# Kernel optimization log

Measured on AMD Instinct MI355X. Metric: run time of the kernel, lower is better.

The kernel has to match this reference:

```python
import jax, jax.numpy as jnp
import numpy as np

B, T, D, H = 64, 257, 1024, 16
F = 4096
R = 16
HD = D // H


def _layer_norm(x, g, b, eps=1e-5):
    mu = x.mean(-1, keepdims=True)
    var = x.var(-1, keepdims=True)
    return (x - mu) / jnp.sqrt(var + eps) * g + b


def _quick_gelu(x):
    return x * jax.nn.sigmoid(1.702 * x)


def _attention(x, Wq, bq, Wk, bk, Wv, bv, Wo, bo):
    scale = HD ** -0.5
    q = (x @ Wq + bq) * scale
    k = x @ Wk + bk
    v = x @ Wv + bv
    q = q.reshape(B, T, H, HD).transpose(0, 2, 1, 3)
    k = k.reshape(B, T, H, HD).transpose(0, 2, 1, 3)
    v = v.reshape(B, T, H, HD).transpose(0, 2, 1, 3)
    attn = jax.nn.softmax(jnp.einsum('bhqd,bhkd->bhqk', q, k), axis=-1)
    o = jnp.einsum('bhqk,bhkd->bhqd', attn, v)
    o = o.transpose(0, 2, 1, 3).reshape(B, T, D)
    return o @ Wo + bo


def _match_indices(metric, r, class_token=True):
    # cosine-normalized bipartite matching (no-grad path in torch; index-only here)
    m = metric / jnp.linalg.norm(metric, axis=-1, keepdims=True)
    a, b = m[:, ::2, :], m[:, 1::2, :]        # [B, ta, D], [B, tb, D]
    scores = jnp.einsum('nac,nbc->nab', a, b)  # [B, ta, tb]
    if class_token:
        scores = scores.at[:, 0, :].set(-jnp.inf)
    node_max = scores.max(-1)
    node_idx = scores.argmax(-1)
    edge_idx = jnp.argsort(-node_max, axis=-1)  # descending
    unm_idx = edge_idx[:, r:]
    src_idx = edge_idx[:, :r]
    dst_idx = jnp.take_along_axis(node_idx, src_idx, axis=-1)
    if class_token:
        unm_idx = jnp.sort(unm_idx, axis=1)
    return unm_idx, src_idx, dst_idx


def _merge_sum(x, unm_idx, src_idx, dst_idx):
    src, dst = x[:, ::2, :], x[:, 1::2, :]
    c = x.shape[-1]
    unm = jnp.take_along_axis(src, unm_idx[..., None], axis=1)       # [B, ta-r, c]
    sel = jnp.take_along_axis(src, src_idx[..., None], axis=1)       # [B, r, c]
    dst = jax.vmap(lambda d, di, sv: d.at[di].add(sv))(dst, dst_idx, sel)
    return jnp.concatenate([unm, dst], axis=1)                       # [B, T-r, c]


def setup_inputs() -> dict:
    key = jax.random.key(0)
    ks = jax.random.split(key, 12)
    s = 0.02
    return {
        'hidden_states': jax.random.normal(ks[0], (B, T, D), jnp.float32),
        'ln1_g': jnp.ones((D,), jnp.float32),
        'ln1_b': jnp.zeros((D,), jnp.float32),
        'Wq': jax.random.normal(ks[1], (D, D), jnp.float32) * s,
        'bq': jnp.zeros((D,), jnp.float32),
        'Wk': jax.random.normal(ks[2], (D, D), jnp.float32) * s,
        'bk': jnp.zeros((D,), jnp.float32),
        'Wv': jax.random.normal(ks[3], (D, D), jnp.float32) * s,
        'bv': jnp.zeros((D,), jnp.float32),
        'Wo': jax.random.normal(ks[4], (D, D), jnp.float32) * s,
        'bo': jnp.zeros((D,), jnp.float32),
        'ln2_g': jnp.ones((D,), jnp.float32),
        'ln2_b': jnp.zeros((D,), jnp.float32),
        'W1': jax.random.normal(ks[5], (D, F), jnp.float32) * s,
        'b1': jnp.zeros((F,), jnp.float32),
        'W2': jax.random.normal(ks[6], (F, D), jnp.float32) * s,
        'b2': jnp.zeros((D,), jnp.float32),
    }


def reference(hidden_states, ln1_g, ln1_b, Wq, bq, Wk, bk, Wv, bv, Wo, bo,
              ln2_g, ln2_b, W1, b1, W2, b2):
    # 1) LN1 + self-attention + residual
    x = hidden_states + _attention(_layer_norm(hidden_states, ln1_g, ln1_b),
                                   Wq, bq, Wk, bk, Wv, bv, Wo, bo)
    # 2) ToMe merge with weighted average (initial size = ones -> merge_wavg)
    metric = jax.lax.stop_gradient(x)
    unm_idx, src_idx, dst_idx = _match_indices(metric, R, class_token=True)
    size = jnp.ones((B, T, 1), x.dtype)
    x = _merge_sum(x * size, unm_idx, src_idx, dst_idx)
    size = _merge_sum(size, unm_idx, src_idx, dst_idx)
    x = x / size
    # 3) LN2 + MLP (quick_gelu) + residual
    h = _layer_norm(x, ln2_g, ln2_b)
    h = _quick_gelu(h @ W1 + b1) @ W2 + b2
    return x + h  # [B, T - R, D]
```

## Files before the change

### kernel.cpp

```cpp
#include <hip/hip_runtime.h>
#include <math.h>

#define BB 64
#define TT 257
#define DD 1024
#define HH 16
#define FF 4096
#define RR 16
#define HDD 64
#define TMM 241
#define M1 (BB*TT)
#define M2 (BB*TMM)
#define NA 129
#define NB 128

typedef float f4v __attribute__((ext_vector_type(4)));
typedef short s8v __attribute__((ext_vector_type(8)));
typedef short s4v __attribute__((ext_vector_type(4)));
typedef unsigned short us;

__device__ __forceinline__ us f2bf(float f){
  unsigned u = __float_as_uint(f);
  u += 0x7fffu + ((u >> 16) & 1u);
  return (us)(u >> 16);
}
__device__ __forceinline__ float bf2f(us h){
  return __uint_as_float(((unsigned)h) << 16);
}
__device__ __forceinline__ void gl16(const us* g, us* l){
  __builtin_amdgcn_global_load_lds((const __attribute__((address_space(1))) void*)g,
                                   (__attribute__((address_space(3))) void*)l, 16, 0, 0);
}

__global__ __launch_bounds__(64) void lnstats_kernel(const float* __restrict__ x,
                                                     float* __restrict__ st)
{
  int row = blockIdx.x, lane = threadIdx.x;
  const float* p = x + (size_t)row * DD;
  float s = 0.0f, sq = 0.0f;
  #pragma unroll
  for (int i = 0; i < 4; i++){
    float4 v = *(const float4*)(p + i * 256 + lane * 4);
    s  += v.x + v.y + v.z + v.w;
    sq += v.x*v.x + v.y*v.y + v.z*v.z + v.w*v.w;
  }
  #pragma unroll
  for (int m = 1; m < 64; m <<= 1){ s += __shfl_xor(s, m); sq += __shfl_xor(sq, m); }
  if (lane == 0){
    float mu  = s * (1.0f / DD);
    float var = sq * (1.0f / DD) - mu * mu;
    st[2*row]     = mu;
    st[2*row + 1] = 1.0f / sqrtf(var + 1e-5f);
  }
}

__global__ __launch_bounds__(256) void lncvt_kernel(const float* __restrict__ x,
    const float* __restrict__ st, const float* __restrict__ g,
    const float* __restrict__ b, us* __restrict__ out)
{
  int row = blockIdx.x, tid = threadIdx.x;
  float mu = st[2*row], rstd = st[2*row + 1];
  float4 xv = *(const float4*)(x + (size_t)row * DD + tid * 4);
  float4 gv = *(const float4*)(g + tid * 4);
  float4 bv = *(const float4*)(b + tid * 4);
  s4v o;
  o[0] = (short)f2bf((xv.x - mu) * rstd * gv.x + bv.x);
  o[1] = (short)f2bf((xv.y - mu) * rstd * gv.y + bv.y);
  o[2] = (short)f2bf((xv.z - mu) * rstd * gv.z + bv.z);
  o[3] = (short)f2bf((xv.w - mu) * rstd * gv.w + bv.w);
  *(s4v*)(out + (size_t)row * DD + tid * 4) = o;
}

__global__ __launch_bounds__(256) void wt_kernel(const float* __restrict__ src,
                                                 us* __restrict__ dhi,
                                                 us* __restrict__ dlo,
                                                 int K, int N)
{
  __shared__ float t[32][33];
  int tx = threadIdx.x, ty = threadIdx.y;
  int n0 = blockIdx.x * 32, k0 = blockIdx.y * 32;
  #pragma unroll
  for (int r = 0; r < 4; r++)
    t[ty + 8*r][tx] = src[(size_t)(k0 + ty + 8*r) * N + n0 + tx];
  __syncthreads();
  #pragma unroll
  for (int r = 0; r < 4; r++){
    float f = t[tx][ty + 8*r];
    us hi = f2bf(f);
    size_t o = (size_t)(n0 + ty + 8*r) * K + k0 + tx;
    dhi[o] = hi;
    if (dlo) dlo[o] = f2bf(f - bf2f(hi));
  }
}

__global__ __launch_bounds__(256) void qkv_kernel(const float* __restrict__ hidden,
    const us* __restrict__ WBh, const us* __restrict__ WBl,
    const float* __restrict__ bq, const float* __restrict__ bk, const float* __restrict__ bv,
    const float* __restrict__ lnstat, const float* __restrict__ lng, const float* __restrict__ lnb,
    us* __restrict__ qhp, us* __restrict__ qlp, us* __restrict__ khp,
    us* __restrict__ klp, us* __restrict__ vhp, us* __restrict__ vlp)
{
  const int M = M1, K = DD;
  __shared__ __align__(16) us Ah[128*32];
  __shared__ __align__(16) us Bh[128*32];
  __shared__ __align__(16) us Al[128*32];
  __shared__ __align__(16) us Bl[128*32];
  int tid = threadIdx.x;
  int m0 = blockIdx.y * 128, n0 = blockIdx.x * 128;
  int lane = tid & 63, w = tid >> 6;
  int wr = w >> 1, wc = w & 1;
  int fr = lane & 15, fq = lane >> 4;
  f4v acc[4][4];
  f4v zero = {0.0f, 0.0f, 0.0f, 0.0f};
  #pragma unroll
  for (int i = 0; i < 4; i++)
    #pragma unroll
    for (int j = 0; j < 4; j++) acc[i][j] = zero;
  int srow = tid >> 1, sseg = (tid & 1) * 16;
  int arow0 = m0 + srow; if (arow0 >= M) arow0 = M - 1;
  float mu = lnstat[2*arow0], rstd = lnstat[2*arow0 + 1];
  int lr = lane >> 2, lc = (lane & 3) * 8;
  int gb0 = n0 + w*32 + lr;

  for (int kk = 0; kk < K; kk += 32){
    {
      const float* ap = hidden + (size_t)arow0 * K + kk + sseg;
      #pragma unroll
      for (int i = 0; i < 4; i++){
        float4 f = *(const float4*)(ap + 4*i);
        float4 gv = *(const float4*)(lng + kk + sseg + 4*i);
        float4 bv2 = *(const float4*)(lnb + kk + sseg + 4*i);
        f.x = (f.x - mu) * rstd * gv.x + bv2.x;
        f.y = (f.y - mu) * rstd * gv.y + bv2.y;
        f.z = (f.z - mu) * rstd * gv.z + bv2.z;
        f.w = (f.w - mu) * rstd * gv.w + bv2.w;
        s4v h;
        h[0] = (short)f2bf(f.x); h[1] = (short)f2bf(f.y);
        h[2] = (short)f2bf(f.z); h[3] = (short)f2bf(f.w);
        *(s4v*)&Ah[srow*32 + sseg + 4*i] = h;
        s4v l;
        l[0] = (short)f2bf(f.x - bf2f((us)h[0]));
        l[1] = (short)f2bf(f.y - bf2f((us)h[1]));
        l[2] = (short)f2bf(f.z - bf2f((us)h[2]));
        l[3] = (short)f2bf(f.w - bf2f((us)h[3]));
        *(s4v*)&Al[srow*32 + sseg + 4*i] = l;
      }
    }
    gl16(WBh + (size_t)gb0 * K + kk + lc,        &Bh[(w*32)*32]);
    gl16(WBh + (size_t)(gb0 + 16) * K + kk + lc, &Bh[(w*32 + 16)*32]);
    gl16(WBl + (size_t)gb0 * K + kk + lc,        &Bl[(w*32)*32]);
    gl16(WBl + (size_t)(gb0 + 16) * K + kk + lc, &Bl[(w*32 + 16)*32]);
    __syncthreads();
    s8v ah[4], bh[4], al[4], bl[4];
    #pragma unroll
    for (int m = 0; m < 4; m++){
      ah[m] = *(const s8v*)&Ah[(wr*64 + m*16 + fr)*32 + fq*8];
      al[m] = *(const s8v*)&Al[(wr*64 + m*16 + fr)*32 + fq*8];
    }
    #pragma unroll
    for (int n = 0; n < 4; n++){
      bh[n] = *(const s8v*)&Bh[(wc*64 + n*16 + fr)*32 + fq*8];
      bl[n] = *(const s8v*)&Bl[(wc*64 + n*16 + fr)*32 + fq*8];
    }
    #pragma unroll
    for (int m = 0; m < 4; m++)
      #pragma unroll
      for (int n = 0; n < 4; n++){
        acc[m][n] = __builtin_amdgcn_mfma_f32_16x16x32_bf16(ah[m], bh[n], acc[m][n], 0, 0, 0);
        acc[m][n] = __builtin_amdgcn_mfma_f32_16x16x32_bf16(ah[m], bl[n], acc[m][n], 0, 0, 0);
        acc[m][n] = __builtin_amdgcn_mfma_f32_16x16x32_bf16(al[m], bh[n], acc[m][n], 0, 0, 0);
      }
    __syncthreads();
  }
  int kind = n0 >> 10;
  const float* bsel = (kind == 0) ? bq : (kind == 1) ? bk : bv;
  us* C0 = (kind == 0) ? qhp : (kind == 1) ? khp : vhp;
  us* C1 = (kind == 0) ? qlp : (kind == 1) ? klp : vlp;
  float scl = (kind == 0) ? 0.125f : 1.0f;
  #pragma unroll
  for (int m = 0; m < 4; m++){
    int grow0 = m0 + wr*64 + m*16 + fq*4;
    #pragma unroll
    for (int n = 0; n < 4; n++){
      int gcol = n0 + wc*64 + n*16 + fr;
      int lcn = gcol & 1023;
      int h2 = lcn >> 6, d2 = lcn & 63;
      float bcol = bsel[lcn];
      #pragma unroll
      for (int i = 0; i < 4; i++){
        int grow = grow0 + i;
        if (grow < M){
          int b2 = grow / 257;
          int t2 = grow - b2 * 257;
          size_t off2 = ((size_t)(b2*16 + h2) * 257 + t2) * 64 + d2;
          float v = (acc[m][n][i] + bcol) * scl;
          us hi = f2bf(v);
          C0[off2] = hi;
          C1[off2] = f2bf(v - bf2f(hi));
        }
      }
    }
  }
}

template<int AMODE, int SPLIT, int EPI>
__global__ __launch_bounds__(256) void gemm2_kernel(const us* __restrict__ Ahp,
    const us* __restrict__ Alp,
    const us* __restrict__ BTh, const us* __restrict__ BTl,
    const float* __restrict__ bias, const float* __restrict__ resid,
    void* __restrict__ C0, int M, int N, int K)
{
  __shared__ __align__(16) us Ah[128*32];
  __shared__ __align__(16) us Bh[128*32];
  __shared__ __align__(16) us Al[SPLIT ? 128*32 : 8];
  __shared__ __align__(16) us Bl[SPLIT ? 128*32 : 8];
  int tid = threadIdx.x;
  int m0 = blockIdx.y * 128, n0 = blockIdx.x * 128;
  int lane = tid & 63, w = tid >> 6;
  int wr = w >> 1, wc = w & 1;
  int fr = lane & 15, fq = lane >> 4;
  f4v acc[4][4];
  f4v zero = {0.0f, 0.0f, 0.0f, 0.0f};
  #pragma unroll
  for (int i = 0; i < 4; i++)
    #pragma unroll
    for (int j = 0; j < 4; j++) acc[i][j] = zero;
  int lr = lane >> 2, lc = (lane & 3) * 8;
  int ga0 = m0 + w*32 + lr;      if (ga0 >= M) ga0 = M - 1;
  int ga1 = m0 + w*32 + 16 + lr; if (ga1 >= M) ga1 = M - 1;
  int gb0 = n0 + w*32 + lr;
  int b2a = ga0 / 257, t2a = ga0 - b2a * 257;
  int b2b = ga1 / 257, t2b = ga1 - b2b * 257;

  for (int kk = 0; kk < K; kk += 32){
    if (AMODE == 1){
      gl16(Ahp + (size_t)ga0 * K + kk + lc, &Ah[(w*32)*32]);
      gl16(Ahp + (size_t)ga1 * K + kk + lc, &Ah[(w*32 + 16)*32]);
      if (SPLIT){
        gl16(Alp + (size_t)ga0 * K + kk + lc, &Al[(w*32)*32]);
        gl16(Alp + (size_t)ga1 * K + kk + lc, &Al[(w*32 + 16)*32]);
      }
    } else {
      int h2 = kk >> 6, d2 = (kk & 63) + lc;
      size_t o0 = ((size_t)(b2a*16 + h2) * 257 + t2a) * 64 + d2;
      size_t o1 = ((size_t)(b2b*16 + h2) * 257 + t2b) * 64 + d2;
      gl16(Ahp + o0, &Ah[(w*32)*32]);
      gl16(Ahp + o1, &Ah[(w*32 + 16)*32]);
      if (SPLIT){
        gl16(Alp + o0, &Al[(w*32)*32]);
        gl16(Alp + o1, &Al[(w*32 + 16)*32]);
      }
    }
    gl16(BTh + (size_t)gb0 * K + kk + lc,        &Bh[(w*32)*32]);
    gl16(BTh + (size_t)(gb0 + 16) * K + kk + lc, &Bh[(w*32 + 16)*32]);
    if (SPLIT){
      gl16(BTl + (size_t)gb0 * K + kk + lc,        &Bl[(w*32)*32]);
      gl16(BTl + (size_t)(gb0 + 16) * K + kk + lc, &Bl[(w*32 + 16)*32]);
    }
    __syncthreads();
    s8v ah[4], bh[4], al[4], bl[4];
    #pragma unroll
    for (int m = 0; m < 4; m++){
      ah[m] = *(const s8v*)&Ah[(wr*64 + m*16 + fr)*32 + fq*8];
      if (SPLIT) al[m] = *(const s8v*)&Al[(wr*64 + m*16 + fr)*32 + fq*8];
    }
    #pragma unroll
    for (int n = 0; n < 4; n++){
      bh[n] = *(const s8v*)&Bh[(wc*64 + n*16 + fr)*32 + fq*8];
      if (SPLIT) bl[n] = *(const s8v*)&Bl[(wc*64 + n*16 + fr)*32 + fq*8];
    }
    #pragma unroll
    for (int m = 0; m < 4; m++)
      #pragma unroll
      for (int n = 0; n < 4; n++){
        acc[m][n] = __builtin_amdgcn_mfma_f32_16x16x32_bf16(ah[m], bh[n], acc[m][n], 0, 0, 0);
        if (SPLIT){
          acc[m][n] = __builtin_amdgcn_mfma_f32_16x16x32_bf16(ah[m], bl[n], acc[m][n], 0, 0, 0);
          acc[m][n] = __builtin_amdgcn_mfma_f32_16x16x32_bf16(al[m], bh[n], acc[m][n], 0, 0, 0);
        }
      }
    __syncthreads();
  }
  #pragma unroll
  for (int m = 0; m < 4; m++){
    int grow0 = m0 + wr*64 + m*16 + fq*4;
    #pragma unroll
    for (int n = 0; n < 4; n++){
      int gcol = n0 + wc*64 + n*16 + fr;
      float bcol = bias[gcol];
      #pragma unroll
      for (int i = 0; i < 4; i++){
        int grow = grow0 + i;
        if (grow < M){
          float v = acc[m][n][i] + bcol;
          size_t off = (size_t)grow * N + gcol;
          if (EPI == 1){
            ((float*)C0)[off] = v + resid[off];
          } else {
            float gq = v / (1.0f + expf(-1.702f * v));
            ((us*)C0)[off] = f2bf(gq);
          }
        }
      }
    }
  }
}

__global__ __launch_bounds__(512, 1) void attn_flash_kernel(
    const us* __restrict__ Qh, const us* __restrict__ Ql,
    const us* __restrict__ Kh, const us* __restrict__ Klo,
    const us* __restrict__ Vh, const us* __restrict__ Vlo,
    us* Oh, us* Ol)
{
  __shared__ __align__(16) us Kl[257 * 128];
  __shared__ __align__(16) us Vl[64 * 640];
  int bh = blockIdx.x;
  const size_t hb = (size_t)bh * 257 * 64;
  int tid = threadIdx.x;
  int l = tid & 63, w = tid >> 6;
  int g = l >> 4, c = l & 15;
  const float NEG = -3.0e38f;

  {
    s8v z8 = {0,0,0,0,0,0,0,0};
    for (int idx = tid; idx < 64*640/8; idx += 512)
      *((s8v*)Vl + idx) = z8;
  }
  __syncthreads();
  for (int idx = tid; idx < 257*8; idx += 512){
    int tok = idx >> 3, ch = idx & 7;
    int sw = (tok & 7) << 4;
    s8v hv = *(const s8v*)(Kh  + hb + (size_t)tok * 64 + ch*8);
    s8v lv = *(const s8v*)(Klo + hb + (size_t)tok * 64 + ch*8);
    char* kr = (char*)Kl + tok * 256;
    *(s8v*)(kr + ((ch*16) ^ sw)) = hv;
    *(s8v*)(kr + 128 + ((ch*16) ^ sw)) = lv;
  }
  for (int idx = tid; idx < 257*8; idx += 512){
    int tok = idx >> 3, ch = idx & 7;
    s8v hv = *(const s8v*)(Vh  + hb + (size_t)tok * 64 + ch*8);
    s8v lv = *(const s8v*)(Vlo + hb + (size_t)tok * 64 + ch*8);
    #pragma unroll
    for (int j = 0; j < 8; j++){
      int d = ch*8 + j;
      char* vr = (char*)Vl + d * 1280;
      int off = (tok * 2) ^ (j << 4);
      *(us*)(vr + off) = (us)hv[j];
      *(us*)(vr + 640 + off) = (us)lv[j];
    }
  }
  __syncthreads();

  for (int qt = w; qt < 17; qt += 8){
    int t0 = qt * 16;
    int qr = t0 + c; if (qr > 256) qr = 256;
    const us* qp  = Qh + hb + (size_t)qr * 64 + g*8;
    const us* qp2 = Ql + hb + (size_t)qr * 64 + g*8;
    s8v qhi[2], qlo[2];
    qhi[0] = *(const s8v*)(qp);       qhi[1] = *(const s8v*)(qp + 32);
    qlo[0] = *(const s8v*)(qp2);      qlo[1] = *(const s8v*)(qp2 + 32);

    float m_run = NEG, l_run = 0.0f;
    f4v o4[4];
    #pragma unroll
    for (int dt = 0; dt < 4; dt++) o4[dt] = (f4v){0.0f, 0.0f, 0.0f, 0.0f};

    #pragma unroll 1
    for (int mck = 0; mck < 9; mck++){
      f4v a0, a1;
      {
        int t = 2*mck;
        int krow = t * 16 + c; if (krow > 256) krow = 256;
        char* kr = (char*)Kl + krow * 256;
        int sw = (krow & 7) << 4;
        s8v khi0 = *(const s8v*)(kr + ((g * 16) ^ sw));
        s8v khi1 = *(const s8v*)(kr + ((64 + g * 16) ^ sw));
        s8v klo0 = *(const s8v*)(kr + 128 + ((g * 16) ^ sw));
        s8v klo1 = *(const s8v*)(kr + 128 + ((64 + g * 16) ^ sw));
        f4v a = {0.0f, 0.0f, 0.0f, 0.0f};
        a = __builtin_amdgcn_mfma_f32_16x16x32_bf16(khi0, qhi[0], a, 0, 0, 0);
        a = __builtin_amdgcn_mfma_f32_16x16x32_bf16(khi1, qhi[1], a, 0, 0, 0);
        a = __builtin_amdgcn_mfma_f32_16x16x32_bf16(khi0, qlo[0], a, 0, 0, 0);
        a = __builtin_amdgcn_mfma_f32_16x16x32_bf16(khi1, qlo[1], a, 0, 0, 0);
        a = __builtin_amdgcn_mfma_f32_16x16x32_bf16(klo0, qhi[0], a, 0, 0, 0);
        a = __builtin_amdgcn_mfma_f32_16x16x32_bf16(klo1, qhi[1], a, 0, 0, 0);
        a0 = a;
      }
      if (mck < 8){
        int t = 2*mck + 1;
        int krow = t * 16 + c; if (krow > 256) krow = 256;
        char* kr = (char*)Kl + krow * 256;
        int sw = (krow & 7) << 4;
        s8v khi0 = *(const s8v*)(kr + ((g * 16) ^ sw));
        s8v khi1 = *(const s8v*)(kr + ((64 + g * 16) ^ sw));
        s8v klo0 = *(const s8v*)(kr + 128 + ((g * 16) ^ sw));
        s8v klo1 = *(const s8v*)(kr + 128 + ((64 + g * 16) ^ sw));
        f4v a = {0.0f, 0.0f, 0.0f, 0.0f};
        a = __builtin_amdgcn_mfma_f32_16x16x32_bf16(khi0, qhi[0], a, 0, 0, 0);
        a = __builtin_amdgcn_mfma_f32_16x16x32_bf16(khi1, qhi[1], a, 0, 0, 0);
        a = __builtin_amdgcn_mfma_f32_16x16x32_bf16(khi0, qlo[0], a, 0, 0, 0);
        a = __builtin_amdgcn_mfma_f32_16x16x32_bf16(khi1, qlo[1], a, 0, 0, 0);
        a = __builtin_amdgcn_mfma_f32_16x16x32_bf16(klo0, qhi[0], a, 0, 0, 0);
        a = __builtin_amdgcn_mfma_f32_16x16x32_bf16(klo1, qhi[1], a, 0, 0, 0);
        a1 = a;
      } else {
        a1 = (f4v){NEG, NEG, NEG, NEG};
        a0[0] = (g == 0) ? a0[0] : NEG;
        a0[1] = NEG; a0[2] = NEG; a0[3] = NEG;
      }
      float cm = fmaxf(fmaxf(fmaxf(a0[0], a0[1]), fmaxf(a0[2], a0[3])),
                       fmaxf(fmaxf(a1[0], a1[1]), fmaxf(a1[2], a1[3])));
      cm = fmaxf(cm, __shfl_xor(cm, 16));
      cm = fmaxf(cm, __shfl_xor(cm, 32));
      float m_new = fmaxf(m_run, cm);
      float scl = __expf(m_run - m_new);
      m_run = m_new;
      l_run *= scl;
      #pragma unroll
      for (int dt = 0; dt < 4; dt++){
        o4[dt][0] *= scl; o4[dt][1] *= scl; o4[dt][2] *= scl; o4[dt][3] *= scl;
      }
      float ls = 0.0f;
      unsigned Ph2[2][2], Pl2[2][2];
      #pragma unroll
      for (int k2 = 0; k2 < 2; k2++){
        float e0 = __expf(a0[2*k2] - m_new), e1 = __expf(a0[2*k2+1] - m_new);
        ls += e0 + e1;
        us h0 = f2bf(e0), h1 = f2bf(e1);
        Ph2[0][k2] = (unsigned)h0 | ((unsigned)h1 << 16);
        Pl2[0][k2] = (unsigned)f2bf(e0 - bf2f(h0)) | ((unsigned)f2bf(e1 - bf2f(h1)) << 16);
        float e2 = __expf(a1[2*k2] - m_new), e3 = __expf(a1[2*k2+1] - m_new);
        ls += e2 + e3;
        us h2 = f2bf(e2), h3 = f2bf(e3);
        Ph2[1][k2] = (unsigned)h2 | ((unsigned)h3 << 16);
        Pl2[1][k2] = (unsigned)f2bf(e2 - bf2f(h2)) | ((unsigned)f2bf(e3 - bf2f(h3)) << 16);
      }
      l_run += ls;
      s8v pbh, pbl;
      #pragma unroll
      for (int ww = 0; ww < 4; ww++){
        int srcl = (((g & 1) * 2 + (ww >> 1)) << 4) | c;
        unsigned h0 = (unsigned)__shfl((int)Ph2[0][ww & 1], srcl, 64);
        unsigned lo0 = (unsigned)__shfl((int)Pl2[0][ww & 1], srcl, 64);
        unsigned h1 = (unsigned)__shfl((int)Ph2[1][ww & 1], srcl, 64);
        unsigned lo1 = (unsigned)__shfl((int)Pl2[1][ww & 1], srcl, 64);
        ((unsigned*)&pbh)[ww] = (g >> 1) ? h1 : h0;
        ((unsigned*)&pbl)[ww] = (g >> 1) ? lo1 : lo0;
      }
      #pragma unroll
      for (int dt = 0; dt < 4; dt++){
        int d = dt * 16 + c;
        char* vr = (char*)Vl + d * 1280;
        int off = (mck * 64 + g * 16) ^ ((d & 7) << 4);
        s8v vh = *(const s8v*)(vr + off);
        s8v vlo = *(const s8v*)(vr + 640 + off);
        o4[dt] = __builtin_amdgcn_mfma_f32_16x16x32_bf16(vh, pbh, o4[dt], 0, 0, 0);
        o4[dt] = __builtin_amdgcn_mfma_f32_16x16x32_bf16(vh, pbl, o4[dt], 0, 0, 0);
        o4[dt] = __builtin_amdgcn_mfma_f32_16x16x32_bf16(vlo, pbh, o4[dt], 0, 0, 0);
      }
    }
    l_run += __shfl_xor(l_run, 16);
    l_run += __shfl_xor(l_run, 32);
    float inv = 1.0f / l_run;
    int qrow = t0 + c;
    if (qrow <= 256){
      us* oph = Oh + hb + (size_t)qrow * 64;
      us* opl = Ol + hb + (size_t)qrow * 64;
      #pragma unroll
      for (int dt = 0; dt < 4; dt++){
        s4v hv4, lv4;
        #pragma unroll
        for (int i = 0; i < 4; i++){
          float ov = o4[dt][i] * inv;
          us hi = f2bf(ov);
          hv4[i] = (short)hi;
          lv4[i] = (short)f2bf(ov - bf2f(hi));
        }
        *(s4v*)(oph + dt*16 + g*4) = hv4;
        *(s4v*)(opl + dt*16 + g*4) = lv4;
      }
    }
  }
}

__global__ __launch_bounds__(64) void norms_kernel(const float* __restrict__ x, float* __restrict__ nrm)
{
  int row = blockIdx.x, lane = threadIdx.x;
  const float* p = x + (size_t)row * DD;
  float sq = 0.0f;
  #pragma unroll
  for (int i = 0; i < 4; i++){
    float4 v = *(const float4*)(p + i * 256 + lane * 4);
    sq += v.x*v.x + v.y*v.y + v.z*v.z + v.w*v.w;
  }
  #pragma unroll
  for (int m = 1; m < 64; m <<= 1) sq += __shfl_xor(sq, m);
  if (lane == 0) nrm[row] = sqrtf(sq);
}

__global__ __launch_bounds__(256) void scores_kernel(const float* __restrict__ x,
                                                     const float* __restrict__ nrm,
                                                     float* __restrict__ sc)
{
  __shared__ __align__(16) float as_[16][1028];
  __shared__ __align__(16) float bs_[16][1028];
  int it = blockIdx.x, b = blockIdx.y;
  int tid = threadIdx.x;
  int rloc = tid >> 4, chunk = tid & 15;
  {
    int i = it * 16 + rloc;
    int tg = (i < NA) ? 2 * i : 2 * (NA - 1);
    const float* p = x + ((size_t)b * TT + tg) * DD + chunk * 64;
    #pragma unroll
    for (int ii = 0; ii < 16; ii++)
      *(float4*)&as_[rloc][chunk * 64 + 4*ii] = *(const float4*)(p + 4*ii);
  }
  for (int jt = 0; jt < 8; jt++){
    __syncthreads();
    {
      int j = jt * 16 + rloc;
      const float* p = x + ((size_t)b * TT + 2*j + 1) * DD + chunk * 64;
      #pragma unroll
      for (int ii = 0; ii < 16; ii++)
        *(float4*)&bs_[rloc][chunk * 64 + 4*ii] = *(const float4*)(p + 4*ii);
    }
    __syncthreads();
    int iloc = tid >> 4, jloc = tid & 15;
    float sum = 0.0f;
    #pragma unroll 8
    for (int cgg = 0; cgg < 1024; cgg += 4){
      float4 av = *(const float4*)&as_[iloc][cgg];
      float4 bvv = *(const float4*)&bs_[jloc][cgg];
      sum += av.x*bvv.x + av.y*bvv.y + av.z*bvv.z + av.w*bvv.w;
    }
    int i = it * 16 + iloc, j = jt * 16 + jloc;
    if (i < NA){
      float val = sum / (nrm[(size_t)b * TT + 2*i] * nrm[(size_t)b * TT + 2*j + 1]);
      sc[((size_t)b * NA + i) * NB + j] = val;
    }
  }
}

__global__ __launch_bounds__(64) void node_kernel(const float* __restrict__ sc,
                                                  float* __restrict__ nmax, int* __restrict__ nidx)
{
  int i = blockIdx.x, b = blockIdx.y, lane = threadIdx.x;
  const float* row = sc + ((size_t)b * NA + i) * NB;
  float v0 = row[lane];
  float v1 = row[lane + 64];
  float bv = v0; int bi = lane;
  if (v1 > bv){ bv = v1; bi = lane + 64; }
  #pragma unroll
  for (int m = 1; m < 64; m <<= 1){
    float ov = __shfl_xor(bv, m);
    int oi = __shfl_xor(bi, m);
    if (ov > bv || (ov == bv && oi < bi)){ bv = ov; bi = oi; }
  }
  if (lane == 0){
    if (i == 0){ nmax[(size_t)b * NA] = -INFINITY; nidx[(size_t)b * NA] = 0; }
    else { nmax[(size_t)b * NA + i] = bv; nidx[(size_t)b * NA + i] = bi; }
  }
}

__global__ __launch_bounds__(256) void rank_kernel(const float* __restrict__ nmax,
    const int* __restrict__ nidx, int* __restrict__ src, int* __restrict__ dst,
    int* __restrict__ unm, int* __restrict__ cnt)
{
  __shared__ float v[NA];
  __shared__ int rk[NA];
  __shared__ int edge[NA];
  __shared__ int cs[NB];
  int b = blockIdx.x, t = threadIdx.x;
  if (t < NA) v[t] = nmax[(size_t)b * NA + t];
  if (t < NB) cs[t] = 0;
  __syncthreads();
  if (t < NA){
    float vt = v[t]; int r = 0;
    for (int i = 0; i < NA; i++){
      float vi = v[i];
      r += (vi > vt) || (vi == vt && i < t);
    }
    rk[t] = r; edge[r] = t;
  }
  __syncthreads();
  if (t < RR){
    int s = edge[t];
    src[b * RR + t] = s;
    int d = nidx[(size_t)b * NA + s];
    dst[b * RR + t] = d;
    atomicAdd(&cs[d], 1);
  }
  if (t < NA && rk[t] >= RR){
    int p = 0;
    for (int i = 0; i < NA; i++) p += (i < t) && (rk[i] >= RR);
    unm[b * (NA - RR) + p] = t;
  }
  __syncthreads();
  if (t < NB) cnt[b * NB + t] = cs[t];
}

__global__ __launch_bounds__(256) void merge_kernel(const float* __restrict__ x,
    const int* __restrict__ src, const int* __restrict__ dst, const int* __restrict__ unm,
    const int* __restrict__ cnt, float* __restrict__ xm)
{
  int u = blockIdx.x, b = blockIdx.y;
  int c = threadIdx.x * 4;
  const float* xb = x + (size_t)b * TT * DD;
  float4 acc;
  if (u < NA - RR){
    int ts = 2 * unm[b * (NA - RR) + u];
    acc = *(const float4*)(xb + (size_t)ts * DD + c);
  } else {
    int j = u - (NA - RR);
    acc = *(const float4*)(xb + (size_t)(2*j + 1) * DD + c);
    #pragma unroll
    for (int k2 = 0; k2 < RR; k2++){
      if (dst[b * RR + k2] == j){
        int ts = 2 * src[b * RR + k2];
        float4 av = *(const float4*)(xb + (size_t)ts * DD + c);
        acc.x += av.x; acc.y += av.y; acc.z += av.z; acc.w += av.w;
      }
    }
    float inv = 1.0f / (float)(1 + cnt[b * NB + j]);
    acc.x *= inv; acc.y *= inv; acc.z *= inv; acc.w *= inv;
  }
  *(float4*)(xm + ((size_t)b * TMM + u) * DD + c) = acc;
}

extern "C" void kernel_launch(void* const* d_in, const int* in_sizes, int n_in,
                              void* d_out, int out_size, void* d_ws, size_t ws_size,
                              hipStream_t stream)
{
  (void)in_sizes; (void)n_in; (void)out_size; (void)ws_size;
  const float* hidden = (const float*)d_in[0];
  const float* ln1_g  = (const float*)d_in[1];
  const float* ln1_b  = (const float*)d_in[2];
  const float* Wq = (const float*)d_in[3];
  const float* bq = (const float*)d_in[4];
  const float* Wk = (const float*)d_in[5];
  const float* bk = (const float*)d_in[6];
  const float* Wv = (const float*)d_in[7];
  const float* bv = (const float*)d_in[8];
  const float* Wo = (const float*)d_in[9];
  const float* bo = (const float*)d_in[10];
  const float* ln2_g = (const float*)d_in[11];
  const float* ln2_b = (const float*)d_in[12];
  const float* W1 = (const float*)d_in[13];
  const float* b1 = (const float*)d_in[14];
  const float* W2 = (const float*)d_in[15];
  const float* b2 = (const float*)d_in[16];

  char* base = (char*)d_ws;
  const size_t PE = (size_t)M1 * DD;
  const size_t PL = PE * sizeof(us);
  us* qh = (us*)base;          us* ql = qh + PE;
  us* kh = (us*)(base + 2*PL); us* kl = kh + PE;
  us* vh = (us*)(base + 4*PL); us* vl = vh + PE;
  us* wts = (us*)(base + 6*PL);
  const size_t WD = (size_t)DD * DD;
  us* wqh = wts;
  us* wkh = wqh + WD;
  us* wvh = wkh + WD;
  us* wql = wvh + WD;
  us* wkl = wql + WD;
  us* wvl = wkl + WD;
  us* woh = wvl + WD;
  us* wol = woh + WD;
  us* w1h = wol + WD;
  us* w2h = w1h + (size_t)DD * FF;
  float* lnst1 = (float*)(w2h + (size_t)FF * DD);
  float* xb = (float*)(base + 2*PL);
  float* nrm   = (float*)(base + 4*PL);
  float* sc    = nrm + M1;
  float* nmaxp = sc + (size_t)BB * NA * NB;
  int*   nidxp = (int*)(nmaxp + BB * NA);
  int*   srcI  = nidxp + BB * NA;
  int*   dstI  = srcI + BB * RR;
  int*   unmI  = dstI + BB * RR;
  int*   cntI  = unmI + BB * (NA - RR);
  us*    xh2   = (us*)(base + 4*PL + (size_t)8*1024*1024);
  float* lnst2 = (float*)(base + 4*PL + (size_t)48*1024*1024);
  float* xm = (float*)d_out;
  us* mid = (us*)base;

  dim3 tb32(32, 8);
  wt_kernel<<<dim3(DD/32, DD/32), tb32, 0, stream>>>(Wq, wqh, wql, DD, DD);
  wt_kernel<<<dim3(DD/32, DD/32), tb32, 0, stream>>>(Wk, wkh, wkl, DD, DD);
  wt_kernel<<<dim3(DD/32, DD/32), tb32, 0, stream>>>(Wv, wvh, wvl, DD, DD);
  wt_kernel<<<dim3(DD/32, DD/32), tb32, 0, stream>>>(Wo, woh, wol, DD, DD);
  wt_kernel<<<dim3(FF/32, DD/32), tb32, 0, stream>>>(W1, w1h, nullptr, DD, FF);
  wt_kernel<<<dim3(DD/32, FF/32), tb32, 0, stream>>>(W2, w2h, nullptr, FF, DD);

  lnstats_kernel<<<M1, 64, 0, stream>>>(hidden, lnst1);

  qkv_kernel<<<dim3(3072/128, (M1 + 127)/128), 256, 0, stream>>>(hidden, wqh, wql,
      bq, bk, bv, lnst1, ln1_g, ln1_b, qh, ql, kh, kl, vh, vl);

  attn_flash_kernel<<<BB*HH, 512, 0, stream>>>(qh, ql, kh, kl, vh, vl, qh, ql);

  gemm2_kernel<2,1,1><<<dim3(DD/128, (M1 + 127)/128), 256, 0, stream>>>(qh, ql, woh, wol,
      bo, hidden, xb, M1, DD, DD);

  norms_kernel<<<M1, 64, 0, stream>>>(xb, nrm);
  scores_kernel<<<dim3(9, BB), 256, 0, stream>>>(xb, nrm, sc);
  node_kernel<<<dim3(NA, BB), 64, 0, stream>>>(sc, nmaxp, nidxp);
  rank_kernel<<<BB, 256, 0, stream>>>(nmaxp, nidxp, srcI, dstI, unmI, cntI);
  merge_kernel<<<dim3(TMM, BB), 256, 0, stream>>>(xb, srcI, dstI, unmI, cntI, xm);

  lnstats_kernel<<<M2, 64, 0, stream>>>(xm, lnst2);
  lncvt_kernel<<<M2, 256, 0, stream>>>(xm, lnst2, ln2_g, ln2_b, xh2);

  gemm2_kernel<1,0,2><<<dim3(FF/128, (M2 + 127)/128), 256, 0, stream>>>(xh2, nullptr, w1h, nullptr,
      b1, nullptr, mid, M2, FF, DD);
  gemm2_kernel<1,0,1><<<dim3(DD/128, (M2 + 127)/128), 256, 0, stream>>>(mid, nullptr, w2h, nullptr,
      b2, xm, (float*)d_out, M2, DD, FF);
}
```

Measured before the change: 1.633 ms.

## Fold LayerNorm1 into QKV weights and apply affine correction in epilogue

LN1's gamma is folded into the transposed QKV weights, and a new kernel precomputes per-column sums g·W and b·W. The QKV GEMM now loads raw hidden states and only splits them into bf16 hi/lo, with no per-element normalization in the K loop. Mean, rstd and beta are applied in the epilogue as rstd*acc - rstd*mu*c1 + c2. This cuts ALU work and gamma/beta loads from the A-tile staging, but it risks precision loss: the raw inputs carry the mean, so the hi/lo split and the mean subtraction after accumulation can cancel catastrophically.

```diff
diff --git a/kernel.cpp b/kernel.cpp
--- a/kernel.cpp
+++ b/kernel.cpp
@@ -74,6 +74,7 @@
 __global__ __launch_bounds__(256) void wt_kernel(const float* __restrict__ src,
                                                  us* __restrict__ dhi,
                                                  us* __restrict__ dlo,
+                                                 const float* __restrict__ gscale,
                                                  int K, int N)
 {
   __shared__ float t[32][33];
@@ -83,9 +84,10 @@
   for (int r = 0; r < 4; r++)
     t[ty + 8*r][tx] = src[(size_t)(k0 + ty + 8*r) * N + n0 + tx];
   __syncthreads();
+  float gs = gscale ? gscale[k0 + tx] : 1.0f;
   #pragma unroll
   for (int r = 0; r < 4; r++){
-    float f = t[tx][ty + 8*r];
+    float f = t[tx][ty + 8*r] * gs;
     us hi = f2bf(f);
     size_t o = (size_t)(n0 + ty + 8*r) * K + k0 + tx;
     dhi[o] = hi;
@@ -93,10 +95,34 @@
   }
 }
 
+__global__ __launch_bounds__(256) void qc_kernel(const float* __restrict__ Wq,
+    const float* __restrict__ Wk, const float* __restrict__ Wv,
+    const float* __restrict__ g, const float* __restrict__ b,
+    float* __restrict__ c1, float* __restrict__ c2)
+{
+  __shared__ float p1[4][64], p2[4][64];
+  int n0 = blockIdx.x * 64;
+  int kind = n0 >> 10, col0 = n0 & 1023;
+  const float* W = (kind == 0) ? Wq : (kind == 1) ? Wk : Wv;
+  int tx = threadIdx.x & 63, ty = threadIdx.x >> 6;
+  float s1 = 0.0f, s2 = 0.0f;
+  for (int k = ty; k < 1024; k += 4){
+    float w = W[(size_t)k * 1024 + col0 + tx];
+    s1 += g[k] * w;
+    s2 += b[k] * w;
+  }
+  p1[ty][tx] = s1; p2[ty][tx] = s2;
+  __syncthreads();
+  if (ty == 0){
+    c1[n0 + tx] = p1[0][tx] + p1[1][tx] + p1[2][tx] + p1[3][tx];
+    c2[n0 + tx] = p2[0][tx] + p2[1][tx] + p2[2][tx] + p2[3][tx];
+  }
+}
+
 __global__ __launch_bounds__(256) void qkv_kernel(const float* __restrict__ hidden,
     const us* __restrict__ WBh, const us* __restrict__ WBl,
     const float* __restrict__ bq, const float* __restrict__ bk, const float* __restrict__ bv,
-    const float* __restrict__ lnstat, const float* __restrict__ lng, const float* __restrict__ lnb,
+    const float* __restrict__ lnstat, const float* __restrict__ c1, const float* __restrict__ c2,
     us* __restrict__ qhp, us* __restrict__ qlp, us* __restrict__ khp,
     us* __restrict__ klp, us* __restrict__ vhp, us* __restrict__ vlp)
 {
@@ -116,35 +142,30 @@
   for (int i = 0; i < 4; i++)
     #pragma unroll
     for (int j = 0; j < 4; j++) acc[i][j] = zero;
-  int srow = tid >> 1, sseg = (tid & 1) * 16;
-  int arow0 = m0 + srow; if (arow0 >= M) arow0 = M - 1;
-  float mu = lnstat[2*arow0], rstd = lnstat[2*arow0 + 1];
+  int sr = tid >> 2, sc4 = (tid & 3) * 8;
+  int ar0 = m0 + sr;       if (ar0 >= M) ar0 = M - 1;
+  int ar1 = m0 + 64 + sr;  if (ar1 >= M) ar1 = M - 1;
   int lr = lane >> 2, lc = (lane & 3) * 8;
   int gb0 = n0 + w*32 + lr;
 
   for (int kk = 0; kk < K; kk += 32){
-    {
-      const float* ap = hidden + (size_t)arow0 * K + kk + sseg;
-      #pragma unroll
-      for (int i = 0; i < 4; i++){
-        float4 f = *(const float4*)(ap + 4*i);
-        float4 gv = *(const float4*)(lng + kk + sseg + 4*i);
-        float4 bv2 = *(const float4*)(lnb + kk + sseg + 4*i);
-        f.x = (f.x - mu) * rstd * gv.x + bv2.x;
-        f.y = (f.y - mu) * rstd * gv.y + bv2.y;
-        f.z = (f.z - mu) * rstd * gv.z + bv2.z;
-        f.w = (f.w - mu) * rstd * gv.w + bv2.w;
-        s4v h;
-        h[0] = (short)f2bf(f.x); h[1] = (short)f2bf(f.y);
-        h[2] = (short)f2bf(f.z); h[3] = (short)f2bf(f.w);
-        *(s4v*)&Ah[srow*32 + sseg + 4*i] = h;
-        s4v l;
-        l[0] = (short)f2bf(f.x - bf2f((us)h[0]));
-        l[1] = (short)f2bf(f.y - bf2f((us)h[1]));
-        l[2] = (short)f2bf(f.z - bf2f((us)h[2]));
-        l[3] = (short)f2bf(f.w - bf2f((us)h[3]));
-        *(s4v*)&Al[srow*32 + sseg + 4*i] = l;
-      }
+    #pragma unroll
+    for (int half = 0; half < 2; half++){
+      int ar = half ? ar1 : ar0;
+      const float* ap = hidden + (size_t)ar * K + kk + sc4;
+      float4 fa = *(const float4*)(ap);
+      float4 fb = *(const float4*)(ap + 4);
+      float fv[8] = {fa.x, fa.y, fa.z, fa.w, fb.x, fb.y, fb.z, fb.w};
+      s8v h, l;
+      #pragma unroll
+      for (int j = 0; j < 8; j++){
+        us hi = f2bf(fv[j]);
+        h[j] = (short)hi;
+        l[j] = (short)f2bf(fv[j] - bf2f(hi));
+      }
+      int lrow = half * 64 + sr;
+      *(s8v*)&Ah[lrow*32 + sc4] = h;
+      *(s8v*)&Al[lrow*32 + sc4] = l;
     }
     gl16(WBh + (size_t)gb0 * K + kk + lc,        &Bh[(w*32)*32]);
     gl16(WBh + (size_t)(gb0 + 16) * K + kk + lc, &Bh[(w*32 + 16)*32]);
@@ -185,15 +206,16 @@
       int gcol = n0 + wc*64 + n*16 + fr;
       int lcn = gcol & 1023;
       int h2 = lcn >> 6, d2 = lcn & 63;
-      float bcol = bsel[lcn];
+      float cc1 = c1[gcol], cc2 = c2[gcol] + bsel[lcn];
       #pragma unroll
       for (int i = 0; i < 4; i++){
         int grow = grow0 + i;
         if (grow < M){
+          float mu = lnstat[2*grow], rstd = lnstat[2*grow + 1];
           int b2 = grow / 257;
           int t2 = grow - b2 * 257;
           size_t off2 = ((size_t)(b2*16 + h2) * 257 + t2) * 64 + d2;
-          float v = (acc[m][n][i] + bcol) * scl;
+          float v = (rstd * acc[m][n][i] - rstd * mu * cc1 + cc2) * scl;
           us hi = f2bf(v);
           C0[off2] = hi;
           C1[off2] = f2bf(v - bf2f(hi));
@@ -669,6 +691,8 @@
   us* w1h = wol + WD;
   us* w2h = w1h + (size_t)DD * FF;
   float* lnst1 = (float*)(w2h + (size_t)FF * DD);
+  float* c1p   = lnst1 + 2 * M1;
+  float* c2p   = c1p + 3072;
   float* xb = (float*)(base + 2*PL);
   float* nrm   = (float*)(base + 4*PL);
   float* sc    = nrm + M1;
@@ -684,17 +708,18 @@
   us* mid = (us*)base;
 
   dim3 tb32(32, 8);
-  wt_kernel<<<dim3(DD/32, DD/32), tb32, 0, stream>>>(Wq, wqh, wql, DD, DD);
-  wt_kernel<<<dim3(DD/32, DD/32), tb32, 0, stream>>>(Wk, wkh, wkl, DD, DD);
-  wt_kernel<<<dim3(DD/32, DD/32), tb32, 0, stream>>>(Wv, wvh, wvl, DD, DD);
-  wt_kernel<<<dim3(DD/32, DD/32), tb32, 0, stream>>>(Wo, woh, wol, DD, DD);
-  wt_kernel<<<dim3(FF/32, DD/32), tb32, 0, stream>>>(W1, w1h, nullptr, DD, FF);
-  wt_kernel<<<dim3(DD/32, FF/32), tb32, 0, stream>>>(W2, w2h, nullptr, FF, DD);
-
+  wt_kernel<<<dim3(DD/32, DD/32), tb32, 0, stream>>>(Wq, wqh, wql, ln1_g, DD, DD);
+  wt_kernel<<<dim3(DD/32, DD/32), tb32, 0, stream>>>(Wk, wkh, wkl, ln1_g, DD, DD);
+  wt_kernel<<<dim3(DD/32, DD/32), tb32, 0, stream>>>(Wv, wvh, wvl, ln1_g, DD, DD);
+  wt_kernel<<<dim3(DD/32, DD/32), tb32, 0, stream>>>(Wo, woh, wol, nullptr, DD, DD);
+  wt_kernel<<<dim3(FF/32, DD/32), tb32, 0, stream>>>(W1, w1h, nullptr, nullptr, DD, FF);
+  wt_kernel<<<dim3(DD/32, FF/32), tb32, 0, stream>>>(W2, w2h, nullptr, nullptr, FF, DD);
+
+  qc_kernel<<<48, 256, 0, stream>>>(Wq, Wk, Wv, ln1_g, ln1_b, c1p, c2p);
   lnstats_kernel<<<M1, 64, 0, stream>>>(hidden, lnst1);
 
   qkv_kernel<<<dim3(3072/128, (M1 + 127)/128), 256, 0, stream>>>(hidden, wqh, wql,
-      bq, bk, bv, lnst1, ln1_g, ln1_b, qh, ql, kh, kl, vh, vl);
+      bq, bk, bv, lnst1, c1p, c2p, qh, ql, kh, kl, vh, vl);
 
   attn_flash_kernel<<<BB*HH, 512, 0, stream>>>(qh, ql, kh, kl, vh, vl, qh, ql);
 
```

Result: slower. 1.724 ms (+5.5%).
